# Optimization experiments

Measured on AMD Instinct MI355X. Metric: run time of the kernel, lower is better.

Reference implementation:

```python
import jax, jax.numpy as jnp
import numpy as np

SPS_AMPLIFY = 1.5
SPS_DAMPEN = 0.3
SPS_DEEP_QUESTION = 0.1
SPS_EXCLAIM = 0.85
SPS_QUESTION = 0.25
SPS_SUPER_EXCLAIM = 0.95

B, S, D = 4, 2048, 1024
NUM_HEADS = 16
HEAD_DIM = D // NUM_HEADS
SCALE = HEAD_DIM ** (-0.5)


def sps_pro(x):
    """Piecewise elementwise modulation based on sigmoid(x) bands."""
    xn = jax.nn.sigmoid(x)
    # bands: xn>0.95 -> 2.0 ; 0.85<xn<=0.95 -> 1.5 ; xn<0.1 -> 0.1 ;
    #        0.1<=xn<0.25 -> 0.3 ; else -> 1.0
    mult = jnp.where(
        xn > SPS_SUPER_EXCLAIM, 2.0,
        jnp.where(xn > SPS_EXCLAIM, SPS_AMPLIFY,
                  jnp.where(xn < SPS_DEEP_QUESTION, 0.1,
                            jnp.where(xn < SPS_QUESTION, SPS_DAMPEN, 1.0))))
    return x * mult


def setup_inputs() -> dict:
    key = jax.random.key(0)
    k0, k1, k2, k3, k4 = jax.random.split(key, 5)
    s = 1.0 / np.sqrt(D)
    return {
        "x": jax.random.normal(k0, (B, S, D), dtype=jnp.float32),
        "W_qkv": jax.random.uniform(k1, (D, 3 * D), dtype=jnp.float32, minval=-s, maxval=s),
        "b_qkv": jax.random.uniform(k2, (3 * D,), dtype=jnp.float32, minval=-s, maxval=s),
        "W_proj": jax.random.uniform(k3, (D, D), dtype=jnp.float32, minval=-s, maxval=s),
        "b_proj": jax.random.uniform(k4, (D,), dtype=jnp.float32, minval=-s, maxval=s),
    }


def reference(x, W_qkv, b_qkv, W_proj, b_proj):
    qkv = jnp.einsum('bsd,de->bse', x, W_qkv) + b_qkv  # [B,S,3D]
    q, k, v = jnp.split(qkv, 3, axis=-1)               # each [B,S,D]
    attn = jnp.einsum('bsd,btd->bst', q, k) * SCALE    # [B,S,S]
    attn = sps_pro(attn)
    attn = jax.nn.softmax(attn, axis=-1)
    out = jnp.einsum('bst,btd->bsd', attn, v)          # [B,S,D]
    out = jnp.einsum('bsd,de->bse', out, W_proj) + b_proj
    return out
```

## Files before the change

kernel.cpp:

```cpp
#include <hip/hip_runtime.h>
#include <hip/hip_bf16.h>
#include <hip/hip_fp16.h>
#include <stdint.h>

typedef __attribute__((ext_vector_type(8))) _Float16 f16x8;
typedef __attribute__((ext_vector_type(4))) float f32x4;

__device__ __forceinline__ void async16(void* lds, const void* g) {
  __builtin_amdgcn_global_load_lds(
      (const __attribute__((address_space(1))) void*)g,
      (__attribute__((address_space(3))) void*)lds, 16, 0, 0);
}

__device__ __forceinline__ uint16_t f2h_u(float f) {
  union { __half h; uint16_t u; } c;
  c.h = __float2half(f);
  return c.u;
}

__global__ __launch_bounds__(256)
void conv_f2h(const float* __restrict__ in, uint16_t* __restrict__ out, int n4) {
  int i = blockIdx.x * 256 + threadIdx.x;
  if (i >= n4) return;
  float4 v = ((const float4*)in)[i];
  ushort4 o;
  o.x = f2h_u(v.x); o.y = f2h_u(v.y); o.z = f2h_u(v.z); o.w = f2h_u(v.w);
  ((ushort4*)out)[i] = o;
}

__global__ __launch_bounds__(256)
void trans_f2h(const float* __restrict__ in, uint16_t* __restrict__ out,
               int ldin, int ldout) {
  __shared__ float t[64][65];
  const int tx = threadIdx.x & 63, ty = threadIdx.x >> 6;
  const int r0 = blockIdx.y * 64, c0 = blockIdx.x * 64;
#pragma unroll
  for (int i = 0; i < 16; ++i)
    t[ty + i * 4][tx] = in[(size_t)(r0 + ty + i * 4) * ldin + c0 + tx];
  __syncthreads();
#pragma unroll
  for (int i = 0; i < 16; ++i)
    out[(size_t)(c0 + ty + i * 4) * ldout + r0 + tx] = f2h_u(t[tx][ty + i * 4]);
}

template <int EPI>
__global__ __launch_bounds__(512, 2)
void gemm_big(const uint16_t* __restrict__ A, const uint16_t* __restrict__ B,
              void* __restrict__ Cv, void* __restrict__ Cv2, void* __restrict__ Cv3,
              const float* __restrict__ bias,
              int nT, int lda, int ldb, int ldc,
              long long strA, long long strB, long long strC) {
  extern __shared__ uint16_t lds_u16[];

  const int gx = gridDim.x, gy = gridDim.y;
  const int nwg = gx * gy * gridDim.z;
  const int fid = blockIdx.x + gx * (blockIdx.y + gy * blockIdx.z);
  const int fs = (fid & 7) * (nwg >> 3) + (fid >> 3);
  const int bx = fs % gx;
  const int by = (fs / gx) % gy;
  const int bz = fs / (gx * gy);

  const int tid = threadIdx.x;
  const int l = tid & 63;
  const int w = tid >> 6;
  const int wm = w >> 2, wn = w & 3;
  const int l15 = l & 15, l4 = l >> 4;
  const int rowBase = bx * 256, colBase = by * 256;
  const uint16_t* Ag = A + (size_t)bz * strA;
  const uint16_t* Bg = B + (size_t)bz * strB;

  const uint16_t* pA[4];
  const uint16_t* pB[4];
#pragma unroll
  for (int u = 0; u < 4; ++u) {
    int c = tid + (u << 9);
    int cs = c ^ ((c >> 3) & 7);
    pA[u] = Ag + (size_t)(rowBase + (cs >> 3)) * lda + (cs & 7) * 8;
    pB[u] = Bg + (size_t)(colBase + (cs >> 3)) * ldb + (cs & 7) * 8;
  }

  f32x4 acc[8][4];
#pragma unroll
  for (int m = 0; m < 8; ++m)
#pragma unroll
    for (int n = 0; n < 4; ++n)
      acc[m][n] = (f32x4){0.f, 0.f, 0.f, 0.f};

#define STAGE(t2, s2)                                                          \
  {                                                                            \
    const int kb_ = (t2) << 6;                                                 \
    uint16_t* dA_ = lds_u16 + (s2) * 32768;                                    \
    uint16_t* dB_ = dA_ + 16384;                                               \
    _Pragma("unroll") for (int u = 0; u < 4; ++u) {                            \
      async16(&dA_[(size_t)(tid + (u << 9)) * 8], pA[u] + kb_);                \
      async16(&dB_[(size_t)(tid + (u << 9)) * 8], pB[u] + kb_);                \
    }                                                                          \
  }

#define ABYTE(r, ks) ((r) * 128 + ((((ks) * 64) + l4 * 16) ^ (((r) & 7) << 4)))

  STAGE(0, 0)
  STAGE(1, 1)
  asm volatile("s_waitcnt vmcnt(8)" ::: "memory");
  __builtin_amdgcn_s_barrier();

  for (int t = 0; t < nT; ++t) {
    const int sl = t & 1;
    const uint16_t* As = lds_u16 + sl * 32768;
    const uint16_t* Bs = As + 16384;
    f16x8 a0[4][2], a1[4][2], b0[2][2], b1[2][2];
#pragma unroll
    for (int mr = 0; mr < 4; ++mr) {
      const int r = wm * 128 + mr * 16 + l15;
#pragma unroll
      for (int ks = 0; ks < 2; ++ks)
        a0[mr][ks] = *(const f16x8*)((const char*)As + ABYTE(r, ks));
    }
#pragma unroll
    for (int nr = 0; nr < 2; ++nr) {
      const int r = wn * 64 + nr * 16 + l15;
#pragma unroll
      for (int ks = 0; ks < 2; ++ks)
        b0[nr][ks] = *(const f16x8*)((const char*)Bs + ABYTE(r, ks));
    }
    __builtin_amdgcn_s_setprio(1);
#pragma unroll
    for (int ks = 0; ks < 2; ++ks)
#pragma unroll
      for (int mr = 0; mr < 4; ++mr)
#pragma unroll
        for (int nr = 0; nr < 2; ++nr)
          acc[mr][nr] = __builtin_amdgcn_mfma_f32_16x16x32_f16(a0[mr][ks], b0[nr][ks], acc[mr][nr], 0, 0, 0);
    __builtin_amdgcn_s_setprio(0);
    __builtin_amdgcn_s_barrier();
#pragma unroll
    for (int nr = 0; nr < 2; ++nr) {
      const int r = wn * 64 + 32 + nr * 16 + l15;
#pragma unroll
      for (int ks = 0; ks < 2; ++ks)
        b1[nr][ks] = *(const f16x8*)((const char*)Bs + ABYTE(r, ks));
    }
    __builtin_amdgcn_s_setprio(1);
#pragma unroll
    for (int ks = 0; ks < 2; ++ks)
#pragma unroll
      for (int mr = 0; mr < 4; ++mr)
#pragma unroll
        for (int nr = 0; nr < 2; ++nr)
          acc[mr][2 + nr] = __builtin_amdgcn_mfma_f32_16x16x32_f16(a0[mr][ks], b1[nr][ks], acc[mr][2 + nr], 0, 0, 0);
    __builtin_amdgcn_s_setprio(0);
    __builtin_amdgcn_s_barrier();
#pragma unroll
    for (int mr = 0; mr < 4; ++mr) {
      const int r = wm * 128 + 64 + mr * 16 + l15;
#pragma unroll
      for (int ks = 0; ks < 2; ++ks)
        a1[mr][ks] = *(const f16x8*)((const char*)As + ABYTE(r, ks));
    }
    __builtin_amdgcn_s_setprio(1);
#pragma unroll
    for (int ks = 0; ks < 2; ++ks)
#pragma unroll
      for (int mr = 0; mr < 4; ++mr)
#pragma unroll
        for (int nr = 0; nr < 2; ++nr)
          acc[4 + mr][2 + nr] = __builtin_amdgcn_mfma_f32_16x16x32_f16(a1[mr][ks], b1[nr][ks], acc[4 + mr][2 + nr], 0, 0, 0);
    __builtin_amdgcn_s_setprio(0);
    __builtin_amdgcn_s_barrier();
    if (t + 2 < nT) STAGE(t + 2, sl)
    __builtin_amdgcn_s_setprio(1);
#pragma unroll
    for (int ks = 0; ks < 2; ++ks)
#pragma unroll
      for (int mr = 0; mr < 4; ++mr)
#pragma unroll
        for (int nr = 0; nr < 2; ++nr)
          acc[4 + mr][nr] = __builtin_amdgcn_mfma_f32_16x16x32_f16(a1[mr][ks], b0[nr][ks], acc[4 + mr][nr], 0, 0, 0);
    __builtin_amdgcn_s_setprio(0);
    if (t + 1 < nT) {
      if (t + 2 < nT) {
        asm volatile("s_waitcnt vmcnt(8)" ::: "memory");
      } else {
        asm volatile("s_waitcnt vmcnt(0)" ::: "memory");
      }
      __builtin_amdgcn_s_barrier();
    }
  }
#undef STAGE
#undef ABYTE

  if (EPI == 0) {
    uint16_t* qd = (uint16_t*)Cv;
    uint16_t* kd = (uint16_t*)Cv2;
    uint16_t* vt = (uint16_t*)Cv3;
#pragma unroll
    for (int ni = 0; ni < 4; ++ni) {
      const int gcol = colBase + wn * 64 + ni * 16 + l15;
      const float bv = bias[gcol];
      if (gcol < 2048) {
        uint16_t* base = (gcol < 1024 ? qd : kd) + (gcol & 1023);
#pragma unroll
        for (int mi = 0; mi < 8; ++mi)
#pragma unroll
          for (int j = 0; j < 4; ++j) {
            const int grow = rowBase + wm * 128 + mi * 16 + l4 * 4 + j;
            base[(size_t)(grow >> 11) * 2097152 + (size_t)(grow & 2047) * 1024] =
                f2h_u(acc[mi][ni][j] + bv);
          }
      } else {
        const int d = gcol - 2048;
#pragma unroll
        for (int mi = 0; mi < 8; ++mi) {
          const int grow0 = rowBase + wm * 128 + mi * 16 + l4 * 4;
          ushort4 o;
          o.x = f2h_u(acc[mi][ni][0] + bv);
          o.y = f2h_u(acc[mi][ni][1] + bv);
          o.z = f2h_u(acc[mi][ni][2] + bv);
          o.w = f2h_u(acc[mi][ni][3] + bv);
          *(ushort4*)&vt[(size_t)(grow0 >> 11) * 2097152 + (size_t)d * 2048 +
                         (grow0 & 2047)] = o;
        }
      }
    }
  } else {
    uint16_t* C = (uint16_t*)Cv + (size_t)bz * strC;
#pragma unroll
    for (int ni = 0; ni < 4; ++ni) {
      const int gcol = colBase + wn * 64 + ni * 16 + l15;
#pragma unroll
      for (int mi = 0; mi < 8; ++mi)
#pragma unroll
        for (int j = 0; j < 4; ++j) {
          const int grow = rowBase + wm * 128 + mi * 16 + l4 * 4 + j;
          float xs = acc[mi][ni][j] * 0.125f;
          float mult = (xs > 2.94443897916644f) ? 2.0f
                     : (xs > 1.73460105538811f) ? 1.5f
                     : (xs < -2.19722457733622f) ? 0.1f
                     : (xs < -1.09861228866811f) ? 0.3f
                                                 : 1.0f;
          C[(size_t)grow * ldc + gcol] = f2h_u(xs * mult);
        }
    }
  }
}

template <int EPI>
__global__ __launch_bounds__(512, 2)
void gemm_sm(const uint16_t* __restrict__ A, const uint16_t* __restrict__ B,
             void* __restrict__ Cv, const float* __restrict__ bias,
             int nT, int lda, int ldb, int ldc,
             long long strA, long long strB, long long strC) {
  extern __shared__ uint16_t lds_u16[];

  const int gx = gridDim.x, gy = gridDim.y;
  const int nwg = gx * gy * gridDim.z;
  const int fid = blockIdx.x + gx * (blockIdx.y + gy * blockIdx.z);
  const int fs = (fid & 7) * (nwg >> 3) + (fid >> 3);
  const int bx = fs % gx;
  const int by = (fs / gx) % gy;
  const int bz = fs / (gx * gy);

  const int tid = threadIdx.x;
  const int l = tid & 63;
  const int w = tid >> 6;
  const int wm = w >> 1, wn = w & 1;
  const int l15 = l & 15, l4 = l >> 4;
  const int rowBase = bx * 256, colBase = by * 128;
  const uint16_t* Ag = A + (size_t)bz * strA;
  const uint16_t* Bg = B + (size_t)bz * strB;

  const uint16_t* pA[4];
  const uint16_t* pB[2];
#pragma unroll
  for (int u = 0; u < 4; ++u) {
    int c = tid + (u << 9);
    int cs = c ^ ((c >> 3) & 7);
    pA[u] = Ag + (size_t)(rowBase + (cs >> 3)) * lda + (cs & 7) * 8;
  }
#pragma unroll
  for (int u = 0; u < 2; ++u) {
    int c = tid + (u << 9);
    int cs = c ^ ((c >> 3) & 7);
    pB[u] = Bg + (size_t)(colBase + (cs >> 3)) * ldb + (cs & 7) * 8;
  }

  f32x4 acc[4][4];
#pragma unroll
  for (int m = 0; m < 4; ++m)
#pragma unroll
    for (int n = 0; n < 4; ++n)
      acc[m][n] = (f32x4){0.f, 0.f, 0.f, 0.f};

#define STAGE(t2, s2)                                                          \
  {                                                                            \
    const int kb_ = (t2) << 6;                                                 \
    uint16_t* dA_ = lds_u16 + (s2) * 24576;                                    \
    uint16_t* dB_ = dA_ + 16384;                                               \
    _Pragma("unroll") for (int u = 0; u < 4; ++u)                              \
        async16(&dA_[(size_t)(tid + (u << 9)) * 8], pA[u] + kb_);              \
    _Pragma("unroll") for (int u = 0; u < 2; ++u)                              \
        async16(&dB_[(size_t)(tid + (u << 9)) * 8], pB[u] + kb_);              \
  }

  STAGE(0, 0)
  STAGE(1, 1)
  asm volatile("s_waitcnt vmcnt(6)" ::: "memory");
  __builtin_amdgcn_s_barrier();

  int sl = 0;
  for (int t = 0; t < nT; ++t) {
    int s2 = sl + 2; if (s2 >= 3) s2 -= 3;
    if (t + 2 < nT) STAGE(t + 2, s2)
    const uint16_t* As = lds_u16 + sl * 24576;
    const uint16_t* Bs = As + 16384;
#pragma unroll
    for (int ks = 0; ks < 2; ++ks) {
      f16x8 af[4], bf[4];
#pragma unroll
      for (int m = 0; m < 4; ++m) {
        const int r = wm * 64 + m * 16 + l15;
        const int byt = r * 128 + ((ks * 64 + l4 * 16) ^ ((r & 7) << 4));
        af[m] = *(const f16x8*)((const char*)As + byt);
      }
#pragma unroll
      for (int n = 0; n < 4; ++n) {
        const int r = wn * 64 + n * 16 + l15;
        const int byt = r * 128 + ((ks * 64 + l4 * 16) ^ ((r & 7) << 4));
        bf[n] = *(const f16x8*)((const char*)Bs + byt);
      }
      __builtin_amdgcn_s_setprio(1);
#pragma unroll
      for (int m = 0; m < 4; ++m)
#pragma unroll
        for (int n = 0; n < 4; ++n)
          acc[m][n] = __builtin_amdgcn_mfma_f32_16x16x32_f16(af[m], bf[n], acc[m][n], 0, 0, 0);
      __builtin_amdgcn_s_setprio(0);
    }
    if (t + 1 < nT) {
      if (t + 2 < nT) {
        asm volatile("s_waitcnt vmcnt(6)" ::: "memory");
      } else {
        asm volatile("s_waitcnt vmcnt(0)" ::: "memory");
      }
      __builtin_amdgcn_s_barrier();
    }
    sl = (sl == 2) ? 0 : sl + 1;
  }
#undef STAGE

  const int orow0 = rowBase + wm * 64 + l4 * 4;
  const int ocol0 = colBase + wn * 64 + l15;
  if (EPI == 3) {
    uint16_t* C = (uint16_t*)Cv + (size_t)bz * strC;
#pragma unroll
    for (int n = 0; n < 4; ++n)
#pragma unroll
      for (int m = 0; m < 4; ++m)
#pragma unroll
        for (int j = 0; j < 4; ++j)
          C[(size_t)(orow0 + m * 16 + j) * ldc + ocol0 + n * 16] = f2h_u(acc[m][n][j]);
  } else {
    float* C = (float*)Cv;
#pragma unroll
    for (int n = 0; n < 4; ++n) {
      const float bv = bias[ocol0 + n * 16];
#pragma unroll
      for (int m = 0; m < 4; ++m)
#pragma unroll
        for (int j = 0; j < 4; ++j)
          C[(size_t)(orow0 + m * 16 + j) * ldc + ocol0 + n * 16] = acc[m][n][j] + bv;
    }
  }
}

__global__ __launch_bounds__(256)
void softmax_rows(uint16_t* __restrict__ P) {
  const size_t row = blockIdx.x;
  uint16_t* p = P + row * 2048;
  const int tid = threadIdx.x;
  uint4 raw = *(const uint4*)(p + tid * 8);
  uint32_t w[4] = {raw.x, raw.y, raw.z, raw.w};
  float v[8];
#pragma unroll
  for (int q = 0; q < 4; ++q) {
    __half2 h = *(__half2*)&w[q];
    float2 f = __half22float2(h);
    v[2 * q] = f.x;
    v[2 * q + 1] = f.y;
  }
  float mx = v[0];
#pragma unroll
  for (int j = 1; j < 8; ++j) mx = fmaxf(mx, v[j]);
#pragma unroll
  for (int o = 32; o > 0; o >>= 1) mx = fmaxf(mx, __shfl_xor(mx, o));
  __shared__ float redm[4], reds[4];
  if ((tid & 63) == 0) redm[tid >> 6] = mx;
  __syncthreads();
  mx = fmaxf(fmaxf(redm[0], redm[1]), fmaxf(redm[2], redm[3]));
  float e[8];
  float se = 0.f;
#pragma unroll
  for (int j = 0; j < 8; ++j) { e[j] = __expf(v[j] - mx); se += e[j]; }
#pragma unroll
  for (int o = 32; o > 0; o >>= 1) se += __shfl_xor(se, o);
  if ((tid & 63) == 0) reds[tid >> 6] = se;
  __syncthreads();
  se = (reds[0] + reds[1]) + (reds[2] + reds[3]);
  const float inv = 1.0f / se;
  uint32_t wo[4];
#pragma unroll
  for (int q = 0; q < 4; ++q) {
    uint16_t a = f2h_u(e[2 * q] * inv);
    uint16_t b = f2h_u(e[2 * q + 1] * inv);
    wo[q] = (uint32_t)a | ((uint32_t)b << 16);
  }
  uint4 ov;
  ov.x = wo[0]; ov.y = wo[1]; ov.z = wo[2]; ov.w = wo[3];
  *(uint4*)(p + tid * 8) = ov;
}

extern "C" void kernel_launch(void* const* d_in, const int* in_sizes, int n_in,
                              void* d_out, int out_size, void* d_ws, size_t ws_size,
                              hipStream_t stream) {
  const float* x     = (const float*)d_in[0];
  const float* Wqkv  = (const float*)d_in[1];
  const float* bqkv  = (const float*)d_in[2];
  const float* Wproj = (const float*)d_in[3];
  const float* bproj = (const float*)d_in[4];
  float* out = (float*)d_out;

  char* ws = (char*)d_ws;
  size_t off = 0;
  auto alloc = [&](size_t bytes) -> void* {
    void* p = ws + off;
    off += (bytes + 255) & ~(size_t)255;
    return p;
  };
  uint16_t* xh    = (uint16_t*)alloc(8192ULL * 1024 * 2);
  uint16_t* WqkvT = (uint16_t*)alloc(3072ULL * 1024 * 2);
  uint16_t* WpT   = (uint16_t*)alloc(1024ULL * 1024 * 2);
  uint16_t* qh    = (uint16_t*)alloc(4ULL * 2048 * 1024 * 2);
  uint16_t* kh    = (uint16_t*)alloc(4ULL * 2048 * 1024 * 2);
  uint16_t* vT    = (uint16_t*)alloc(4ULL * 1024 * 2048 * 2);
  uint16_t* Pm    = (uint16_t*)alloc(4ULL * 2048 * 2048 * 2);
  uint16_t* ao    = xh;

  conv_f2h<<<8192, 256, 0, stream>>>(x, xh, 2097152);
  trans_f2h<<<dim3(48, 16), 256, 0, stream>>>(Wqkv, WqkvT, 3072, 1024);
  trans_f2h<<<dim3(16, 16), 256, 0, stream>>>(Wproj, WpT, 1024, 1024);
  gemm_big<0><<<dim3(32, 12, 1), 512, 131072, stream>>>(
      xh, WqkvT, qh, kh, vT, bqkv, 16, 1024, 1024, 0, 0, 0, 0);
  gemm_big<1><<<dim3(8, 8, 4), 512, 131072, stream>>>(
      qh, kh, Pm, nullptr, nullptr, nullptr, 16, 1024, 1024, 2048,
      2097152LL, 2097152LL, 4194304LL);
  softmax_rows<<<8192, 256, 0, stream>>>(Pm);
  gemm_sm<3><<<dim3(8, 8, 4), 512, 147456, stream>>>(
      Pm, vT, ao, nullptr, 32, 2048, 2048, 1024,
      4194304LL, 2097152LL, 2097152LL);
  gemm_sm<4><<<dim3(32, 8, 1), 512, 147456, stream>>>(
      ao, WpT, out, bproj, 16, 1024, 1024, 1024, 0, 0, 0);
}
```

Measured before the change: 222.9 us.

## Restructure 256x256 GEMM main loop into 8-phase half-tile interleaved prefetch

Replaces the per-k-tile double-buffered loop in the QKV and QK^T GEMM with a two-tile-unrolled, eight-phase schedule. Global-to-LDS loads are split into half-tile pieces for A and B, and each piece is issued between the MFMA phases, so the memory traffic is spread across the compute instead of arriving in one burst. The goal is better overlap of loads with matrix math and fewer stalls at the barrier. It adds more barriers, and nT must be even. The waitcnt accounting is also trickier and easy to get wrong.

```diff
diff --git a/kernel.cpp b/kernel.cpp
--- a/kernel.cpp
+++ b/kernel.cpp
@@ -45,11 +45,11 @@
 
 template <int EPI>
 __global__ __launch_bounds__(512, 2)
-void gemm_big(const uint16_t* __restrict__ A, const uint16_t* __restrict__ B,
-              void* __restrict__ Cv, void* __restrict__ Cv2, void* __restrict__ Cv3,
-              const float* __restrict__ bias,
-              int nT, int lda, int ldb, int ldc,
-              long long strA, long long strB, long long strC) {
+void gemm8p(const uint16_t* __restrict__ A, const uint16_t* __restrict__ B,
+            void* __restrict__ Cv, void* __restrict__ Cv2, void* __restrict__ Cv3,
+            const float* __restrict__ bias,
+            int nT, int lda, int ldb, int ldc,
+            long long strA, long long strB, long long strC) {
   extern __shared__ uint16_t lds_u16[];
 
   const int gx = gridDim.x, gy = gridDim.y;
@@ -69,14 +69,17 @@
   const uint16_t* Ag = A + (size_t)bz * strA;
   const uint16_t* Bg = B + (size_t)bz * strB;
 
-  const uint16_t* pA[4];
-  const uint16_t* pB[4];
-#pragma unroll
-  for (int u = 0; u < 4; ++u) {
+  const uint16_t* sA[2][2];
+  const uint16_t* sB[2][2];
+#pragma unroll
+  for (int u = 0; u < 2; ++u) {
     int c = tid + (u << 9);
     int cs = c ^ ((c >> 3) & 7);
-    pA[u] = Ag + (size_t)(rowBase + (cs >> 3)) * lda + (cs & 7) * 8;
-    pB[u] = Bg + (size_t)(colBase + (cs >> 3)) * ldb + (cs & 7) * 8;
+    int row = cs >> 3, kc = (cs & 7) * 8;
+    sA[0][u] = Ag + (size_t)(rowBase + row) * lda + kc;
+    sA[1][u] = Ag + (size_t)(rowBase + 128 + row) * lda + kc;
+    sB[0][u] = Bg + (size_t)(colBase + row) * ldb + kc;
+    sB[1][u] = Bg + (size_t)(colBase + 128 + row) * ldb + kc;
   }
 
   f32x4 acc[8][4];
@@ -86,108 +89,95 @@
     for (int n = 0; n < 4; ++n)
       acc[m][n] = (f32x4){0.f, 0.f, 0.f, 0.f};
 
-#define STAGE(t2, s2)                                                          \
+#define SH_A(buf, h, koff)                                                     \
   {                                                                            \
-    const int kb_ = (t2) << 6;                                                 \
-    uint16_t* dA_ = lds_u16 + (s2) * 32768;                                    \
-    uint16_t* dB_ = dA_ + 16384;                                               \
-    _Pragma("unroll") for (int u = 0; u < 4; ++u) {                            \
-      async16(&dA_[(size_t)(tid + (u << 9)) * 8], pA[u] + kb_);                \
-      async16(&dB_[(size_t)(tid + (u << 9)) * 8], pB[u] + kb_);                \
-    }                                                                          \
-  }
-
-#define ABYTE(r, ks) ((r) * 128 + ((((ks) * 64) + l4 * 16) ^ (((r) & 7) << 4)))
-
-  STAGE(0, 0)
-  STAGE(1, 1)
-  asm volatile("s_waitcnt vmcnt(8)" ::: "memory");
-  __builtin_amdgcn_s_barrier();
-
-  for (int t = 0; t < nT; ++t) {
-    const int sl = t & 1;
-    const uint16_t* As = lds_u16 + sl * 32768;
-    const uint16_t* Bs = As + 16384;
+    const uint32_t d_ = (buf)*32768u + (h)*8192u;                              \
+    async16(&lds_u16[d_ + (size_t)tid * 8], sA[h][0] + (koff));                \
+    async16(&lds_u16[d_ + (size_t)(tid + 512) * 8], sA[h][1] + (koff));        \
+  }
+#define SH_B(buf, h, koff)                                                     \
+  {                                                                            \
+    const uint32_t d_ = (buf)*32768u + 16384u + (h)*8192u;                     \
+    async16(&lds_u16[d_ + (size_t)tid * 8], sB[h][0] + (koff));                \
+    async16(&lds_u16[d_ + (size_t)(tid + 512) * 8], sB[h][1] + (koff));        \
+  }
+#define RD_A(dst, buf, mh)                                                     \
+  _Pragma("unroll") for (int mr = 0; mr < 4; ++mr) {                           \
+    const int lr = (mh)*64 + mr * 16 + l15;                                    \
+    const char* hb = (const char*)lds_u16 + (buf)*65536 + wm * 16384;          \
+    _Pragma("unroll") for (int ks = 0; ks < 2; ++ks)                           \
+      dst[mr][ks] = *(const f16x8*)(hb + lr * 128 +                            \
+                    ((ks * 64 + l4 * 16) ^ ((lr & 7) << 4)));                  \
+  }
+#define RD_B(dst, buf, nh)                                                     \
+  _Pragma("unroll") for (int nr = 0; nr < 2; ++nr) {                           \
+    const int lr = (wn & 1) * 64 + (nh)*32 + nr * 16 + l15;                    \
+    const char* hb = (const char*)lds_u16 + (buf)*65536 + 32768 +              \
+                     (wn >> 1) * 16384;                                        \
+    _Pragma("unroll") for (int ks = 0; ks < 2; ++ks)                           \
+      dst[nr][ks] = *(const f16x8*)(hb + lr * 128 +                            \
+                    ((ks * 64 + l4 * 16) ^ ((lr & 7) << 4)));                  \
+  }
+#define MM(m0, n0, AF, BF)                                                     \
+  __builtin_amdgcn_s_setprio(1);                                               \
+  _Pragma("unroll") for (int ks = 0; ks < 2; ++ks)                             \
+  _Pragma("unroll") for (int mr = 0; mr < 4; ++mr)                             \
+  _Pragma("unroll") for (int nr = 0; nr < 2; ++nr)                             \
+    acc[(m0) + mr][(n0) + nr] = __builtin_amdgcn_mfma_f32_16x16x32_f16(        \
+        AF[mr][ks], BF[nr][ks], acc[(m0) + mr][(n0) + nr], 0, 0, 0);           \
+  __builtin_amdgcn_s_setprio(0);
+#define VMC(n) asm volatile("s_waitcnt vmcnt(" #n ")" ::: "memory");
+#define BAR() __builtin_amdgcn_s_barrier();
+
+  SH_A(0, 0, 0) SH_A(0, 1, 0) SH_B(0, 0, 0) SH_B(0, 1, 0)
+  SH_B(1, 0, 64) SH_B(1, 1, 64)
+  VMC(4)
+  BAR()
+
+  const int nIter = nT >> 1;
+  for (int i = 0; i < nIter; ++i) {
+    const int e2 = 2 * i + 2, o = 2 * i + 1, o2 = 2 * i + 3;
+    const int ke2 = e2 << 6, ko = o << 6, ko2 = o2 << 6;
     f16x8 a0[4][2], a1[4][2], b0[2][2], b1[2][2];
-#pragma unroll
-    for (int mr = 0; mr < 4; ++mr) {
-      const int r = wm * 128 + mr * 16 + l15;
-#pragma unroll
-      for (int ks = 0; ks < 2; ++ks)
-        a0[mr][ks] = *(const f16x8*)((const char*)As + ABYTE(r, ks));
-    }
-#pragma unroll
-    for (int nr = 0; nr < 2; ++nr) {
-      const int r = wn * 64 + nr * 16 + l15;
-#pragma unroll
-      for (int ks = 0; ks < 2; ++ks)
-        b0[nr][ks] = *(const f16x8*)((const char*)Bs + ABYTE(r, ks));
-    }
-    __builtin_amdgcn_s_setprio(1);
-#pragma unroll
-    for (int ks = 0; ks < 2; ++ks)
-#pragma unroll
-      for (int mr = 0; mr < 4; ++mr)
-#pragma unroll
-        for (int nr = 0; nr < 2; ++nr)
-          acc[mr][nr] = __builtin_amdgcn_mfma_f32_16x16x32_f16(a0[mr][ks], b0[nr][ks], acc[mr][nr], 0, 0, 0);
-    __builtin_amdgcn_s_setprio(0);
-    __builtin_amdgcn_s_barrier();
-#pragma unroll
-    for (int nr = 0; nr < 2; ++nr) {
-      const int r = wn * 64 + 32 + nr * 16 + l15;
-#pragma unroll
-      for (int ks = 0; ks < 2; ++ks)
-        b1[nr][ks] = *(const f16x8*)((const char*)Bs + ABYTE(r, ks));
-    }
-    __builtin_amdgcn_s_setprio(1);
-#pragma unroll
-    for (int ks = 0; ks < 2; ++ks)
-#pragma unroll
-      for (int mr = 0; mr < 4; ++mr)
-#pragma unroll
-        for (int nr = 0; nr < 2; ++nr)
-          acc[mr][2 + nr] = __builtin_amdgcn_mfma_f32_16x16x32_f16(a0[mr][ks], b1[nr][ks], acc[mr][2 + nr], 0, 0, 0);
-    __builtin_amdgcn_s_setprio(0);
-    __builtin_amdgcn_s_barrier();
-#pragma unroll
-    for (int mr = 0; mr < 4; ++mr) {
-      const int r = wm * 128 + 64 + mr * 16 + l15;
-#pragma unroll
-      for (int ks = 0; ks < 2; ++ks)
-        a1[mr][ks] = *(const f16x8*)((const char*)As + ABYTE(r, ks));
-    }
-    __builtin_amdgcn_s_setprio(1);
-#pragma unroll
-    for (int ks = 0; ks < 2; ++ks)
-#pragma unroll
-      for (int mr = 0; mr < 4; ++mr)
-#pragma unroll
-        for (int nr = 0; nr < 2; ++nr)
-          acc[4 + mr][2 + nr] = __builtin_amdgcn_mfma_f32_16x16x32_f16(a1[mr][ks], b1[nr][ks], acc[4 + mr][2 + nr], 0, 0, 0);
-    __builtin_amdgcn_s_setprio(0);
-    __builtin_amdgcn_s_barrier();
-    if (t + 2 < nT) STAGE(t + 2, sl)
-    __builtin_amdgcn_s_setprio(1);
-#pragma unroll
-    for (int ks = 0; ks < 2; ++ks)
-#pragma unroll
-      for (int mr = 0; mr < 4; ++mr)
-#pragma unroll
-        for (int nr = 0; nr < 2; ++nr)
-          acc[4 + mr][nr] = __builtin_amdgcn_mfma_f32_16x16x32_f16(a1[mr][ks], b0[nr][ks], acc[4 + mr][nr], 0, 0, 0);
-    __builtin_amdgcn_s_setprio(0);
-    if (t + 1 < nT) {
-      if (t + 2 < nT) {
-        asm volatile("s_waitcnt vmcnt(8)" ::: "memory");
-      } else {
-        asm volatile("s_waitcnt vmcnt(0)" ::: "memory");
-      }
-      __builtin_amdgcn_s_barrier();
-    }
-  }
-#undef STAGE
-#undef ABYTE
+    RD_A(a0, 0, 0) RD_B(b0, 0, 0)
+    SH_A(1, 0, ko)
+    BAR()
+    MM(0, 0, a0, b0)
+    RD_B(b1, 0, 1)
+    SH_A(1, 1, ko)
+    BAR()
+    MM(0, 2, a0, b1)
+    RD_A(a1, 0, 1)
+    if (e2 < nT) SH_B(0, 0, ke2)
+    BAR()
+    MM(4, 2, a1, b1)
+    if (e2 < nT) { SH_B(0, 1, ke2) VMC(4) } else { VMC(0) }
+    BAR()
+    MM(4, 0, a1, b0)
+    RD_A(a0, 1, 0) RD_B(b0, 1, 0)
+    if (e2 < nT) SH_A(0, 0, ke2)
+    BAR()
+    MM(0, 0, a0, b0)
+    RD_B(b1, 1, 1)
+    if (e2 < nT) SH_A(0, 1, ke2)
+    BAR()
+    MM(0, 2, a0, b1)
+    RD_A(a1, 1, 1)
+    if (o2 < nT) SH_B(1, 0, ko2)
+    BAR()
+    MM(4, 2, a1, b1)
+    if (o2 < nT) { SH_B(1, 1, ko2) }
+    if (i + 1 < nIter) { if (o2 < nT) { VMC(4) } else { VMC(0) } }
+    BAR()
+    MM(4, 0, a1, b0)
+  }
+#undef SH_A
+#undef SH_B
+#undef RD_A
+#undef RD_B
+#undef MM
+#undef VMC
+#undef BAR
 
   if (EPI == 0) {
     uint16_t* qd = (uint16_t*)Cv;
@@ -448,9 +438,9 @@
   conv_f2h<<<8192, 256, 0, stream>>>(x, xh, 2097152);
   trans_f2h<<<dim3(48, 16), 256, 0, stream>>>(Wqkv, WqkvT, 3072, 1024);
   trans_f2h<<<dim3(16, 16), 256, 0, stream>>>(Wproj, WpT, 1024, 1024);
-  gemm_big<0><<<dim3(32, 12, 1), 512, 131072, stream>>>(
+  gemm8p<0><<<dim3(32, 12, 1), 512, 131072, stream>>>(
       xh, WqkvT, qh, kh, vT, bqkv, 16, 1024, 1024, 0, 0, 0, 0);
-  gemm_big<1><<<dim3(8, 8, 4), 512, 131072, stream>>>(
+  gemm8p<1><<<dim3(8, 8, 4), 512, 131072, stream>>>(
       qh, kh, Pm, nullptr, nullptr, nullptr, 16, 1024, 1024, 2048,
       2097152LL, 2097152LL, 4194304LL);
   softmax_rows<<<8192, 256, 0, stream>>>(Pm);
```

After: 214.7 us. 3.6% less time.
